# Performance work log

Hardware: AMD Instinct MI355X
Metric: run time of the kernel (lower is better)

## Reference

```python
import jax, jax.numpy as jnp
import numpy as np

B, N, F_IN, OUT_DIM, H = 8, 2048, 128, 256, 4
D = OUT_DIM // H  # head dim = 64
NEG_SLOPE = 0.2


def setup_inputs() -> dict:
    key = jax.random.key(0)
    k_a, k_x, k_w, k_s, k_d = jax.random.split(key, 5)
    A = jax.random.randint(k_a, (B, N, N), 0, 2).astype(jnp.float32)
    # ensure self-loops so no softmax row is fully masked (-inf -> NaN)
    eye = jnp.eye(N, dtype=jnp.float32)
    A = jnp.maximum(A, eye[None, :, :])
    X = jax.random.normal(k_x, (B, N, F_IN), dtype=jnp.float32)
    # xavier-uniform-like scales
    w_lim = float(np.sqrt(6.0 / (F_IN + OUT_DIM)))
    a_lim = float(np.sqrt(6.0 / (H + D)))
    W = jax.random.uniform(k_w, (OUT_DIM, F_IN), minval=-w_lim, maxval=w_lim, dtype=jnp.float32)
    a_src = jax.random.uniform(k_s, (H, D), minval=-a_lim, maxval=a_lim, dtype=jnp.float32)
    a_dst = jax.random.uniform(k_d, (H, D), minval=-a_lim, maxval=a_lim, dtype=jnp.float32)
    return {"A": A, "X": X, "W": W, "a_src": a_src, "a_dst": a_dst}


def reference(A, X, W, a_src, a_dst):
    b, n, _ = X.shape
    h, d = a_src.shape
    # X_trans = W(X); torch Linear: X @ W.T, W: (out_dim, in_dim)
    X_split = (X @ W.T).reshape(b, n, h, d)  # (b, n, h, d)
    attn_src = jnp.einsum('bnhd,hd->bnh', X_split, a_src)
    attn_dst = jnp.einsum('bnhd,hd->bnh', X_split, a_dst)
    # (b, n, n, h) dense score tensor
    attn = attn_src[:, :, None, :] + attn_dst[:, None, :, :]
    attn = jnp.where(attn >= 0, attn, NEG_SLOPE * attn)  # leaky_relu(0.2)
    attn = jnp.where(A[..., None] == 0, -jnp.inf, attn)
    attn = jax.nn.softmax(attn, axis=2)
    # torch.einsum('bnnk,bnkd->bnkd') with repeated 'n' -> DIAGONAL of attn,
    # elementwise-scaled features (faithful to original code).
    diag = jnp.einsum('bnnh->bnh', attn)  # (b, n, h): self-attention weights
    out = (diag[..., None] * X_split).reshape(b, n, h * d)
    return out
```

## Files before the change

### kernel.cpp

```cpp
#include <hip/hip_runtime.h>
#include <hip/hip_bf16.h>

#define B_   8
#define N_   2048
#define FIN  128
#define OUTD 256
#define H_   4
#define LOG2E 1.44269504088896340736f

typedef __bf16 bf16x8 __attribute__((ext_vector_type(8)));
typedef float  f32x4  __attribute__((ext_vector_type(4)));

__global__ __launch_bounds__(256) void conv_bf16(const float* __restrict__ X,
                                                 const float* __restrict__ W,
                                                 unsigned short* __restrict__ Xb,
                                                 unsigned short* __restrict__ Wb) {
    const int NX4 = (B_ * N_ * FIN) / 4;
    int i = blockIdx.x * 256 + threadIdx.x;
    const float4* src;
    ushort4* dst;
    int idx;
    if (i < NX4) { src = (const float4*)X; dst = (ushort4*)Xb; idx = i; }
    else         { src = (const float4*)W; dst = (ushort4*)Wb; idx = i - NX4; }
    float4 v = src[idx];
    __hip_bfloat16 b0 = __float2bfloat16(v.x);
    __hip_bfloat16 b1 = __float2bfloat16(v.y);
    __hip_bfloat16 b2 = __float2bfloat16(v.z);
    __hip_bfloat16 b3 = __float2bfloat16(v.w);
    ushort4 o;
    o.x = *(unsigned short*)&b0;
    o.y = *(unsigned short*)&b1;
    o.z = *(unsigned short*)&b2;
    o.w = *(unsigned short*)&b3;
    dst[idx] = o;
}

__global__ __launch_bounds__(256) void gemm_bf16(const unsigned short* __restrict__ Xb,
                                                 const unsigned short* __restrict__ Wb,
                                                 float* __restrict__ Xt) {
    int r0   = blockIdx.x * 16;
    int wave = threadIdx.x >> 6;
    int lane = threadIdx.x & 63;
    int c0   = (blockIdx.y * 4 + wave) * 16;
    int m = lane & 15, q = lane >> 4;

    const bf16x8* Arow = (const bf16x8*)(Xb + (size_t)(r0 + m) * FIN);
    const bf16x8* Brow = (const bf16x8*)(Wb + (size_t)(c0 + m) * FIN);
    f32x4 acc = {0.f, 0.f, 0.f, 0.f};
#pragma unroll
    for (int kc = 0; kc < 4; ++kc) {
        bf16x8 af = Arow[kc * 4 + q];
        bf16x8 bf = Brow[kc * 4 + q];
        acc = __builtin_amdgcn_mfma_f32_16x16x32_bf16(af, bf, acc, 0, 0, 0);
    }
    float* outp = Xt + (size_t)(r0 + q * 4) * OUTD + c0 + m;
#pragma unroll
    for (int reg = 0; reg < 4; ++reg)
        outp[(size_t)reg * OUTD] = acc[reg];
}

__global__ __launch_bounds__(256) void st_kernel(const float* __restrict__ Xt,
                                                 const float* __restrict__ a_src,
                                                 const float* __restrict__ a_dst,
                                                 float* __restrict__ s_arr,
                                                 float* __restrict__ t_arr) {
    int row  = blockIdx.x * 4 + (threadIdx.x >> 6);
    int lane = threadIdx.x & 63;
    const float* xr = Xt + (size_t)row * OUTD;
#pragma unroll
    for (int h = 0; h < H_; ++h) {
        float v  = xr[h * 64 + lane];
        float vs = v * a_src[h * 64 + lane];
        float vd = v * a_dst[h * 64 + lane];
#pragma unroll
        for (int off = 32; off > 0; off >>= 1) {
            vs += __shfl_down(vs, off);
            vd += __shfl_down(vd, off);
        }
        if (lane == 0) {
            s_arr[(size_t)row * H_ + h] = vs * LOG2E;
            t_arr[(size_t)row * H_ + h] = vd * LOG2E;
        }
    }
}

__global__ __launch_bounds__(256) void gat_main(const float* __restrict__ A,
                                                const float* __restrict__ s_arr,
                                                const float* __restrict__ t_arr,
                                                float* __restrict__ out) {
    __shared__ float t_lds[N_ * H_];
    __shared__ float diag_lds[16][H_];

    int b  = blockIdx.x >> 7;
    int rt = blockIdx.x & 127;
    int r0 = rt * 16;
    int tid = threadIdx.x;

    {
        const float4* tsrc = (const float4*)(t_arr + (size_t)b * N_ * H_);
        float4* tdst = (float4*)t_lds;
        for (int i = tid; i < (N_ * H_) / 4; i += 256) tdst[i] = tsrc[i];
    }
    __syncthreads();

    int r  = tid >> 4;
    int lj = tid & 15;
    int gi = r0 + r;

    f32x4 s4 = *(const f32x4*)(s_arr + ((size_t)b * N_ + gi) * H_);
    const float* Arow = A + ((size_t)b * N_ + gi) * N_;

    float acc0 = 0.f, acc1 = 0.f, acc2 = 0.f, acc3 = 0.f;
    for (int it = 0; it < N_ / 64; ++it) {
        int j = it * 64 + lj * 4;
        float4 a4 = *(const float4*)(Arow + j);
#pragma unroll
        for (int jj = 0; jj < 4; ++jj) {
            f32x4 t4 = ((const f32x4*)t_lds)[j + jj];
            float aj = (jj == 0) ? a4.x : (jj == 1) ? a4.y : (jj == 2) ? a4.z : a4.w;
            float y0 = s4[0] + t4[0]; y0 = fmaxf(y0, 0.2f * y0); acc0 = fmaf(aj, exp2f(y0), acc0);
            float y1 = s4[1] + t4[1]; y1 = fmaxf(y1, 0.2f * y1); acc1 = fmaf(aj, exp2f(y1), acc1);
            float y2 = s4[2] + t4[2]; y2 = fmaxf(y2, 0.2f * y2); acc2 = fmaf(aj, exp2f(y2), acc2);
            float y3 = s4[3] + t4[3]; y3 = fmaxf(y3, 0.2f * y3); acc3 = fmaf(aj, exp2f(y3), acc3);
        }
    }
#pragma unroll
    for (int mk = 8; mk > 0; mk >>= 1) {
        acc0 += __shfl_xor(acc0, mk);
        acc1 += __shfl_xor(acc1, mk);
        acc2 += __shfl_xor(acc2, mk);
        acc3 += __shfl_xor(acc3, mk);
    }
    if (lj == 0) {
        f32x4 ti = ((const f32x4*)t_lds)[gi];
        float y, e;
        y = s4[0] + ti[0]; y = fmaxf(y, 0.2f * y); e = exp2f(y); diag_lds[r][0] = e / acc0;
        y = s4[1] + ti[1]; y = fmaxf(y, 0.2f * y); e = exp2f(y); diag_lds[r][1] = e / acc1;
        y = s4[2] + ti[2]; y = fmaxf(y, 0.2f * y); e = exp2f(y); diag_lds[r][2] = e / acc2;
        y = s4[3] + ti[3]; y = fmaxf(y, 0.2f * y); e = exp2f(y); diag_lds[r][3] = e / acc3;
    }
    __syncthreads();

    float* orow = out + ((size_t)b * N_ + gi) * OUTD;
#pragma unroll
    for (int ii = 0; ii < 4; ++ii) {
        int c = lj * 4 + ii * 64;
        float4 v = *(float4*)(orow + c);
        float dg = diag_lds[r][ii];
        v.x *= dg; v.y *= dg; v.z *= dg; v.w *= dg;
        *(float4*)(orow + c) = v;
    }
}

extern "C" void kernel_launch(void* const* d_in, const int* in_sizes, int n_in,
                              void* d_out, int out_size, void* d_ws, size_t ws_size,
                              hipStream_t stream) {
    const float* A     = (const float*)d_in[0];
    const float* X     = (const float*)d_in[1];
    const float* W     = (const float*)d_in[2];
    const float* a_src = (const float*)d_in[3];
    const float* a_dst = (const float*)d_in[4];
    float* out = (float*)d_out;

    char* ws = (char*)d_ws;
    unsigned short* Xb = (unsigned short*)ws;
    unsigned short* Wb = (unsigned short*)(ws + 4194304);
    float* s_arr = (float*)(ws + 4259840);
    float* t_arr = (float*)(ws + 4521984);

    conv_bf16<<<2080, 256, 0, stream>>>(X, W, Xb, Wb);
    gemm_bf16<<<dim3(1024, 4), 256, 0, stream>>>(Xb, Wb, out);
    st_kernel<<<4096, 256, 0, stream>>>(out, a_src, a_dst, s_arr, t_arr);
    gat_main<<<1024, 256, 0, stream>>>(A, s_arr, t_arr, out);
}
```

Before: 243.7 us.

## Fuse bf16 conversion, projection GEMM and score reduction into one kernel

Removes the separate fp32-to-bf16 conversion kernel and the attention-score kernel. The GEMM now converts X and W to bf16 in registers and computes the per-head src/dst dot products straight from the MFMA accumulators, using shuffles plus an LDS reduction across waves. The grid is reorganized so each block covers one head for 16 rows. This cuts two launches and the round trips through Xb/Wb and Xt, at the cost of re-reading fp32 X once per head. The main kernel also stores t in planar LDS layout so it can use vector loads per head.

```diff
diff --git a/kernel.cpp b/kernel.cpp
--- a/kernel.cpp
+++ b/kernel.cpp
@@ -10,77 +10,85 @@
 
 typedef __bf16 bf16x8 __attribute__((ext_vector_type(8)));
 typedef float  f32x4  __attribute__((ext_vector_type(4)));
+typedef unsigned short u16x8 __attribute__((ext_vector_type(8)));
 
-__global__ __launch_bounds__(256) void conv_bf16(const float* __restrict__ X,
-                                                 const float* __restrict__ W,
-                                                 unsigned short* __restrict__ Xb,
-                                                 unsigned short* __restrict__ Wb) {
-    const int NX4 = (B_ * N_ * FIN) / 4;
-    int i = blockIdx.x * 256 + threadIdx.x;
-    const float4* src;
-    ushort4* dst;
-    int idx;
-    if (i < NX4) { src = (const float4*)X; dst = (ushort4*)Xb; idx = i; }
-    else         { src = (const float4*)W; dst = (ushort4*)Wb; idx = i - NX4; }
-    float4 v = src[idx];
-    __hip_bfloat16 b0 = __float2bfloat16(v.x);
-    __hip_bfloat16 b1 = __float2bfloat16(v.y);
-    __hip_bfloat16 b2 = __float2bfloat16(v.z);
-    __hip_bfloat16 b3 = __float2bfloat16(v.w);
-    ushort4 o;
-    o.x = *(unsigned short*)&b0;
-    o.y = *(unsigned short*)&b1;
-    o.z = *(unsigned short*)&b2;
-    o.w = *(unsigned short*)&b3;
-    dst[idx] = o;
+__device__ __forceinline__ bf16x8 to_bf16x8(float4 a, float4 b) {
+    u16x8 u;
+    __hip_bfloat16 t;
+    t = __float2bfloat16(a.x); u[0] = *(unsigned short*)&t;
+    t = __float2bfloat16(a.y); u[1] = *(unsigned short*)&t;
+    t = __float2bfloat16(a.z); u[2] = *(unsigned short*)&t;
+    t = __float2bfloat16(a.w); u[3] = *(unsigned short*)&t;
+    t = __float2bfloat16(b.x); u[4] = *(unsigned short*)&t;
+    t = __float2bfloat16(b.y); u[5] = *(unsigned short*)&t;
+    t = __float2bfloat16(b.z); u[6] = *(unsigned short*)&t;
+    t = __float2bfloat16(b.w); u[7] = *(unsigned short*)&t;
+    return __builtin_bit_cast(bf16x8, u);
 }
 
-__global__ __launch_bounds__(256) void gemm_bf16(const unsigned short* __restrict__ Xb,
-                                                 const unsigned short* __restrict__ Wb,
-                                                 float* __restrict__ Xt) {
-    int r0   = blockIdx.x * 16;
-    int wave = threadIdx.x >> 6;
-    int lane = threadIdx.x & 63;
-    int c0   = (blockIdx.y * 4 + wave) * 16;
-    int m = lane & 15, q = lane >> 4;
+__global__ __launch_bounds__(256) void gemm_st(const float* __restrict__ X,
+                                               const float* __restrict__ W,
+                                               const float* __restrict__ a_src,
+                                               const float* __restrict__ a_dst,
+                                               float* __restrict__ Xt,
+                                               float* __restrict__ s_arr,
+                                               float* __restrict__ t_arr) {
+    __shared__ float redS[4][4][4];
+    __shared__ float redT[4][4][4];
 
-    const bf16x8* Arow = (const bf16x8*)(Xb + (size_t)(r0 + m) * FIN);
-    const bf16x8* Brow = (const bf16x8*)(Wb + (size_t)(c0 + m) * FIN);
+    const int h    = blockIdx.x;
+    const int r0   = blockIdx.y * 16;
+    const int wave = threadIdx.x >> 6;
+    const int lane = threadIdx.x & 63;
+    const int m = lane & 15, q = lane >> 4;
+    const int c0 = h * 64 + wave * 16;
+
+    const float4* Xrow = (const float4*)(X + (size_t)(r0 + m) * FIN);
+    const float4* Wrow = (const float4*)(W + (size_t)(c0 + m) * FIN);
+
     f32x4 acc = {0.f, 0.f, 0.f, 0.f};
 #pragma unroll
     for (int kc = 0; kc < 4; ++kc) {
-        bf16x8 af = Arow[kc * 4 + q];
-        bf16x8 bf = Brow[kc * 4 + q];
+        bf16x8 af = to_bf16x8(Xrow[kc * 8 + 2 * q], Xrow[kc * 8 + 2 * q + 1]);
+        bf16x8 bf = to_bf16x8(Wrow[kc * 8 + 2 * q], Wrow[kc * 8 + 2 * q + 1]);
         acc = __builtin_amdgcn_mfma_f32_16x16x32_bf16(af, bf, acc, 0, 0, 0);
     }
+
     float* outp = Xt + (size_t)(r0 + q * 4) * OUTD + c0 + m;
 #pragma unroll
     for (int reg = 0; reg < 4; ++reg)
         outp[(size_t)reg * OUTD] = acc[reg];
-}
 
-__global__ __launch_bounds__(256) void st_kernel(const float* __restrict__ Xt,
-                                                 const float* __restrict__ a_src,
-                                                 const float* __restrict__ a_dst,
-                                                 float* __restrict__ s_arr,
-                                                 float* __restrict__ t_arr) {
-    int row  = blockIdx.x * 4 + (threadIdx.x >> 6);
-    int lane = threadIdx.x & 63;
-    const float* xr = Xt + (size_t)row * OUTD;
+    const int ch = wave * 16 + m;
+    float as = a_src[h * 64 + ch];
+    float ad = a_dst[h * 64 + ch];
+    float ps[4], pt[4];
 #pragma unroll
-    for (int h = 0; h < H_; ++h) {
-        float v  = xr[h * 64 + lane];
-        float vs = v * a_src[h * 64 + lane];
-        float vd = v * a_dst[h * 64 + lane];
+    for (int reg = 0; reg < 4; ++reg) {
+        ps[reg] = acc[reg] * as;
+        pt[reg] = acc[reg] * ad;
 #pragma unroll
-        for (int off = 32; off > 0; off >>= 1) {
-            vs += __shfl_down(vs, off);
-            vd += __shfl_down(vd, off);
+        for (int mk = 1; mk < 16; mk <<= 1) {
+            ps[reg] += __shfl_xor(ps[reg], mk);
+            pt[reg] += __shfl_xor(pt[reg], mk);
         }
-        if (lane == 0) {
-            s_arr[(size_t)row * H_ + h] = vs * LOG2E;
-            t_arr[(size_t)row * H_ + h] = vd * LOG2E;
+    }
+    if (m == 0) {
+#pragma unroll
+        for (int reg = 0; reg < 4; ++reg) {
+            redS[wave][q][reg] = ps[reg];
+            redT[wave][q][reg] = pt[reg];
         }
+    }
+    __syncthreads();
+    if (threadIdx.x < 16) {
+        int rr = threadIdx.x;
+        int qq = rr >> 2, reg = rr & 3;
+        float s = redS[0][qq][reg] + redS[1][qq][reg] + redS[2][qq][reg] + redS[3][qq][reg];
+        float t = redT[0][qq][reg] + redT[1][qq][reg] + redT[2][qq][reg] + redT[3][qq][reg];
+        size_t row = (size_t)r0 + rr;
+        s_arr[row * H_ + h] = s * LOG2E;
+        t_arr[row * H_ + h] = t * LOG2E;
     }
 }
 
@@ -88,40 +96,46 @@
                                                 const float* __restrict__ s_arr,
                                                 const float* __restrict__ t_arr,
                                                 float* __restrict__ out) {
-    __shared__ float t_lds[N_ * H_];
+    __shared__ float t_pl[H_][N_];
     __shared__ float diag_lds[16][H_];
 
-    int b  = blockIdx.x >> 7;
-    int rt = blockIdx.x & 127;
-    int r0 = rt * 16;
-    int tid = threadIdx.x;
+    const int b  = blockIdx.x >> 7;
+    const int rt = blockIdx.x & 127;
+    const int r0 = rt * 16;
+    const int tid = threadIdx.x;
 
-    {
-        const float4* tsrc = (const float4*)(t_arr + (size_t)b * N_ * H_);
-        float4* tdst = (float4*)t_lds;
-        for (int i = tid; i < (N_ * H_) / 4; i += 256) tdst[i] = tsrc[i];
+    const f32x4* tsrc = (const f32x4*)(t_arr + (size_t)b * N_ * H_);
+    for (int i = tid; i < N_; i += 256) {
+        f32x4 tv = tsrc[i];
+        t_pl[0][i] = tv[0];
+        t_pl[1][i] = tv[1];
+        t_pl[2][i] = tv[2];
+        t_pl[3][i] = tv[3];
     }
     __syncthreads();
 
-    int r  = tid >> 4;
-    int lj = tid & 15;
-    int gi = r0 + r;
+    const int r  = tid >> 4;
+    const int lj = tid & 15;
+    const int gi = r0 + r;
 
     f32x4 s4 = *(const f32x4*)(s_arr + ((size_t)b * N_ + gi) * H_);
     const float* Arow = A + ((size_t)b * N_ + gi) * N_;
 
     float acc0 = 0.f, acc1 = 0.f, acc2 = 0.f, acc3 = 0.f;
     for (int it = 0; it < N_ / 64; ++it) {
-        int j = it * 64 + lj * 4;
-        float4 a4 = *(const float4*)(Arow + j);
+        const int j0 = it * 64 + lj * 4;
+        f32x4 a4 = *(const f32x4*)(Arow + j0);
+        f32x4 t0 = *(const f32x4*)&t_pl[0][j0];
+        f32x4 t1 = *(const f32x4*)&t_pl[1][j0];
+        f32x4 t2 = *(const f32x4*)&t_pl[2][j0];
+        f32x4 t3 = *(const f32x4*)&t_pl[3][j0];
 #pragma unroll
         for (int jj = 0; jj < 4; ++jj) {
-            f32x4 t4 = ((const f32x4*)t_lds)[j + jj];
-            float aj = (jj == 0) ? a4.x : (jj == 1) ? a4.y : (jj == 2) ? a4.z : a4.w;
-            float y0 = s4[0] + t4[0]; y0 = fmaxf(y0, 0.2f * y0); acc0 = fmaf(aj, exp2f(y0), acc0);
-            float y1 = s4[1] + t4[1]; y1 = fmaxf(y1, 0.2f * y1); acc1 = fmaf(aj, exp2f(y1), acc1);
-            float y2 = s4[2] + t4[2]; y2 = fmaxf(y2, 0.2f * y2); acc2 = fmaf(aj, exp2f(y2), acc2);
-            float y3 = s4[3] + t4[3]; y3 = fmaxf(y3, 0.2f * y3); acc3 = fmaf(aj, exp2f(y3), acc3);
+            float aj = a4[jj];
+            float y0 = s4[0] + t0[jj]; y0 = fmaxf(y0, 0.2f * y0); acc0 = fmaf(aj, exp2f(y0), acc0);
+            float y1 = s4[1] + t1[jj]; y1 = fmaxf(y1, 0.2f * y1); acc1 = fmaf(aj, exp2f(y1), acc1);
+            float y2 = s4[2] + t2[jj]; y2 = fmaxf(y2, 0.2f * y2); acc2 = fmaf(aj, exp2f(y2), acc2);
+            float y3 = s4[3] + t3[jj]; y3 = fmaxf(y3, 0.2f * y3); acc3 = fmaf(aj, exp2f(y3), acc3);
         }
     }
 #pragma unroll
@@ -132,12 +146,11 @@
         acc3 += __shfl_xor(acc3, mk);
     }
     if (lj == 0) {
-        f32x4 ti = ((const f32x4*)t_lds)[gi];
         float y, e;
-        y = s4[0] + ti[0]; y = fmaxf(y, 0.2f * y); e = exp2f(y); diag_lds[r][0] = e / acc0;
-        y = s4[1] + ti[1]; y = fmaxf(y, 0.2f * y); e = exp2f(y); diag_lds[r][1] = e / acc1;
-        y = s4[2] + ti[2]; y = fmaxf(y, 0.2f * y); e = exp2f(y); diag_lds[r][2] = e / acc2;
-        y = s4[3] + ti[3]; y = fmaxf(y, 0.2f * y); e = exp2f(y); diag_lds[r][3] = e / acc3;
+        y = s4[0] + t_pl[0][gi]; y = fmaxf(y, 0.2f * y); e = exp2f(y); diag_lds[r][0] = e / acc0;
+        y = s4[1] + t_pl[1][gi]; y = fmaxf(y, 0.2f * y); e = exp2f(y); diag_lds[r][1] = e / acc1;
+        y = s4[2] + t_pl[2][gi]; y = fmaxf(y, 0.2f * y); e = exp2f(y); diag_lds[r][2] = e / acc2;
+        y = s4[3] + t_pl[3][gi]; y = fmaxf(y, 0.2f * y); e = exp2f(y); diag_lds[r][3] = e / acc3;
     }
     __syncthreads();
 
@@ -163,13 +176,9 @@
     float* out = (float*)d_out;
 
     char* ws = (char*)d_ws;
-    unsigned short* Xb = (unsigned short*)ws;
-    unsigned short* Wb = (unsigned short*)(ws + 4194304);
-    float* s_arr = (float*)(ws + 4259840);
-    float* t_arr = (float*)(ws + 4521984);
+    float* s_arr = (float*)ws;
+    float* t_arr = (float*)(ws + 262144);
 
-    conv_bf16<<<2080, 256, 0, stream>>>(X, W, Xb, Wb);
-    gemm_bf16<<<dim3(1024, 4), 256, 0, stream>>>(Xb, Wb, out);
-    st_kernel<<<4096, 256, 0, stream>>>(out, a_src, a_dst, s_arr, t_arr);
+    gemm_st<<<dim3(4, 1024), 256, 0, stream>>>(X, W, a_src, a_dst, out, s_arr, t_arr);
     gat_main<<<1024, 256, 0, stream>>>(A, s_arr, t_arr, out);
 }
```

New measurement: 243.8 us. About the same (+0.0%).
